# Kernel optimization log

Measured on AMD Instinct MI355X. Metric: run time of the kernel, lower is better.

## Reference

```python
import jax, jax.numpy as jnp
import numpy as np

FORGET_RADIX = 10
HIDDEN_RADIX = 23
LN2 = float(np.log(2.0))
MAX_FORGET = 0.875
BATCH, IN_SIZE, H_SIZE = 8192, 1024, 2048
G = H_SIZE // 2  # group size (h_size // 2)


def setup_inputs() -> dict:
    key = jax.random.key(0)
    ks = jax.random.split(key, 6)
    x = jax.random.normal(ks[0], (BATCH, IN_SIZE), dtype=jnp.float32)
    # hidden is a fixed-point (radix 23) int state; values correspond to floats in (-0.125, 0.125)
    hidden = jax.random.randint(ks[1], (BATCH, H_SIZE), -(2**20), 2**20, dtype=jnp.int32)

    def lin(k, fan_in, fan_out):
        kw, kb = jax.random.split(k)
        s = 1.0 / np.sqrt(fan_in)
        W = jax.random.uniform(kw, (fan_in, fan_out), jnp.float32, -s, s)
        b = jax.random.uniform(kb, (fan_out,), jnp.float32, -s, s)
        return W, b

    W_zr1, b_zr1 = lin(ks[2], IN_SIZE + G, H_SIZE)
    W_g1, b_g1 = lin(ks[3], IN_SIZE + G, G)
    W_zr2, b_zr2 = lin(ks[4], IN_SIZE + G, H_SIZE)
    W_g2, b_g2 = lin(ks[5], IN_SIZE + G, G)
    return {"x": x, "hidden": hidden,
            "W_zr1": W_zr1, "b_zr1": b_zr1, "W_g1": W_g1, "b_g1": b_g1,
            "W_zr2": W_zr2, "b_zr2": b_zr2, "W_g2": W_g2, "b_g2": b_g2,
            "slice_dim": 0}


def _to_float(h_fix, radix):
    # ConvertToFloat: fixed-point int -> float
    return h_fix.astype(jnp.float32) / np.float32(2.0 ** radix)


def _to_fixed(v, radix):
    # ConvertToFixed: float -> fixed-point int (truncation toward zero, like Tensor.int())
    return jnp.trunc(v * np.float32(2.0 ** radix)).astype(jnp.int64)


def reference(x, hidden, W_zr1, b_zr1, W_g1, b_g1, W_zr2, b_zr2, W_g2, b_g2, slice_dim):
    h = hidden.astype(jnp.int64)  # widen so h * z_fix (up to ~2^34) does not overflow
    h1, h2 = h[:, :G], h[:, G:]

    # ---- group 1 update (reads h2) ----
    h2_fl = _to_float(h2, HIDDEN_RADIX)
    zr1 = jax.nn.sigmoid(jnp.concatenate([x, h2_fl], axis=1) @ W_zr1 + b_zr1)
    z1, r1 = zr1[:, :G], zr1[:, G:]
    z1 = MAX_FORGET * z1 + (1.0 - MAX_FORGET)
    g1 = jnp.tanh(jnp.concatenate([x, r1 * h2_fl], axis=1) @ W_g1 + b_g1)
    z1_fix = jnp.maximum(_to_fixed(z1, FORGET_RADIX), 1)  # EnsureNotForgetAll
    h1 = jnp.floor_divide(h1 * z1_fix, 2 ** FORGET_RADIX)  # FixedMultiply, buf=None, mask=1
    h1 = h1 + _to_fixed((1.0 - z1) * g1, HIDDEN_RADIX)     # + MaskFixedMultiply(update1, 1)

    # ---- group 2 update (reads updated h1) ----
    h1_fl = _to_float(h1, HIDDEN_RADIX)
    zr2 = jax.nn.sigmoid(jnp.concatenate([x, h1_fl], axis=1) @ W_zr2 + b_zr2)
    z2, r2 = zr2[:, :G], zr2[:, G:]
    z2 = MAX_FORGET * z2 + (1.0 - MAX_FORGET)
    g2 = jnp.tanh(jnp.concatenate([x, r2 * h1_fl], axis=1) @ W_g2 + b_g2)
    z2_fix = jnp.maximum(_to_fixed(z2, FORGET_RADIX), 1)
    h2 = jnp.floor_divide(h2 * z2_fix, 2 ** FORGET_RADIX)
    h2 = h2 + _to_fixed((1.0 - z2) * g2, HIDDEN_RADIX)

    recurrent_hidden = jnp.concatenate([h1, h2], axis=1).astype(jnp.int32)
    output_hidden = recurrent_hidden.astype(jnp.float32) / np.float32(2.0 ** HIDDEN_RADIX)

    optimal_bits = (jnp.sum(-jnp.log(z1[:, slice_dim:]) / LN2)
                    + jnp.sum(-jnp.log(z2) / LN2)
                    + 32.0 * slice_dim * x.shape[0])
    return recurrent_hidden, output_hidden, optimal_bits
```

## Files before the change

### kernel.cpp

```cpp
#include <hip/hip_runtime.h>
#include <hip/hip_bf16.h>

#define BATCH   8192
#define IN_SZ   1024
#define HSZ     2048
#define GG      1024
#define KTOT    2048

typedef __hip_bfloat16 bf16;
typedef __attribute__((ext_vector_type(8))) short  short8;
typedef __attribute__((ext_vector_type(4))) float  floatx4;

typedef __attribute__((address_space(1))) const void gvoid_t;
typedef __attribute__((address_space(3))) void       lvoid_t;

__device__ __forceinline__ void async_ld16(void* lds, const void* g) {
  __builtin_amdgcn_global_load_lds((gvoid_t*)g, (lvoid_t*)lds, 16, 0, 0);
}

__global__ void prep_all(const float* __restrict__ x, bf16* __restrict__ xb,
                         const int* __restrict__ hidden, bf16* __restrict__ hf,
                         float* accp,
                         const float* __restrict__ W_zr1, const float* __restrict__ W_g1,
                         const float* __restrict__ W_zr2, const float* __restrict__ W_g2,
                         bf16* __restrict__ wt_zr1, bf16* __restrict__ wt_g1,
                         bf16* __restrict__ wt_zr2, bf16* __restrict__ wt_g2) {
  int b = blockIdx.x;
  int t = threadIdx.x;
  if (b < 3072) {
    const float* W; bf16* Wt; int N; int tb = b;
    if (tb < 1024)      { W = W_zr1; Wt = wt_zr1; N = 2048; }
    else if (tb < 1536) { W = W_g1;  Wt = wt_g1;  N = 1024; tb -= 1024; }
    else if (tb < 2560) { W = W_zr2; Wt = wt_zr2; N = 2048; tb -= 1536; }
    else                { W = W_g2;  Wt = wt_g2;  N = 1024; tb -= 2560; }
    int ntn = N >> 6;
    int k0 = (tb / ntn) * 64, n0 = (tb % ntn) * 64;
    __shared__ float tile[64][65];
    int kk = t >> 4, nn = (t & 15) * 4;
#pragma unroll
    for (int s = 0; s < 4; ++s) {
      int row = kk + s * 16;
      float4 v = *(const float4*)&W[(size_t)(k0 + row) * N + n0 + nn];
      tile[row][nn + 0] = v.x; tile[row][nn + 1] = v.y;
      tile[row][nn + 2] = v.z; tile[row][nn + 3] = v.w;
    }
    __syncthreads();
    int k8 = (t & 7) * 8;
#pragma unroll
    for (int s = 0; s < 2; ++s) {
      int nl = (t >> 3) + s * 32;
      bf16 vals[8];
#pragma unroll
      for (int u = 0; u < 8; ++u) vals[u] = __float2bfloat16(tile[k8 + u][nl]);
      *(short8*)&Wt[(size_t)(n0 + nl) * KTOT + k0 + k8] = *(short8*)vals;
    }
  } else {
    int idx = (b - 3072) * 256 + t;
    int i = idx * 4;
    float4 xv = *(const float4*)(x + i);
    xb[i + 0] = __float2bfloat16(xv.x);
    xb[i + 1] = __float2bfloat16(xv.y);
    xb[i + 2] = __float2bfloat16(xv.z);
    xb[i + 3] = __float2bfloat16(xv.w);
    int m = i >> 10, j = i & 1023;
    int4 hv = *(const int4*)(hidden + m * HSZ + GG + j);
    const float sc = 1.0f / 8388608.0f;
    hf[i + 0] = __float2bfloat16((float)hv.x * sc);
    hf[i + 1] = __float2bfloat16((float)hv.y * sc);
    hf[i + 2] = __float2bfloat16((float)hv.z * sc);
    hf[i + 3] = __float2bfloat16((float)hv.w * sc);
    if (idx == 0) *accp = 0.0f;
  }
}

template<int BM, int MI>
__device__ __forceinline__ void gemm_mainloop(const bf16* __restrict__ Aleft,
                                              const bf16* __restrict__ Aright,
                                              const bf16* __restrict__ Bt,
                                              bf16* As, bf16* Bs,
                                              int m0, int n0, floatx4 (&acc)[MI][4]) {
  int t = threadIdx.x;
  int r = t >> 2;
  int c2 = (t & 3) ^ ((t >> 3) & 3);
  int lane = t & 63;
  int q = lane >> 4, r16 = lane & 15;
  int w = t >> 6;
  int wm = w & 1, wn = w >> 1;
  int swz = q ^ ((r16 >> 1) & 3);

  const size_t arow0 = (size_t)(m0 + r) * IN_SZ;
  const size_t arow1 = (size_t)(m0 + r + 64) * IN_SZ;
  const size_t brow0 = (size_t)(n0 + r) * KTOT;
  const size_t brow1 = (size_t)(n0 + r + 64) * KTOT;
  bf16* lA0 = As + t * 8;
  bf16* lA1 = As + 64 * 32 + t * 8;
  bf16* lB0 = Bs + t * 8;
  bf16* lB1 = Bs + 64 * 32 + t * 8;
  const bf16* aRd = As + (wm * (BM / 2) + r16) * 32 + swz * 8;
  const bf16* bRd = Bs + (wn * 64 + r16) * 32 + swz * 8;

  for (int kb = 0; kb < KTOT / 32; ++kb) {
    int kt = kb * 32;
    const bf16* asrc; int kloc;
    if (kt < IN_SZ) { asrc = Aleft;  kloc = kt; }
    else            { asrc = Aright; kloc = kt - IN_SZ; }
    int ac = kloc + c2 * 8;
    async_ld16(lA0, asrc + arow0 + ac);
    if (BM == 128) async_ld16(lA1, asrc + arow1 + ac);
    int bc = kt + c2 * 8;
    async_ld16(lB0, Bt + brow0 + bc);
    async_ld16(lB1, Bt + brow1 + bc);
    __syncthreads();
    short8 af[MI], bfr[4];
#pragma unroll
    for (int i = 0; i < MI; ++i) af[i]  = *(const short8*)(const void*)(aRd + i * 16 * 32);
#pragma unroll
    for (int j = 0; j < 4; ++j)  bfr[j] = *(const short8*)(const void*)(bRd + j * 16 * 32);
#pragma unroll
    for (int i = 0; i < MI; ++i)
#pragma unroll
      for (int j = 0; j < 4; ++j)
        acc[i][j] = __builtin_amdgcn_mfma_f32_16x16x32_bf16(af[i], bfr[j], acc[i][j], 0, 0, 0);
    __syncthreads();
  }
}

__global__ void gemm_zr(const bf16* __restrict__ xb, const bf16* __restrict__ hfp,
                        const bf16* __restrict__ Bt, const float* __restrict__ bias,
                        bf16* __restrict__ zbuf, bf16* __restrict__ rh,
                        const int* __restrict__ slice_ptr, int use_slice,
                        float* __restrict__ accp) {
  __shared__ bf16 As[128 * 32];
  __shared__ bf16 Bs[128 * 32];
  floatx4 acc[4][4];
#pragma unroll
  for (int i = 0; i < 4; ++i)
#pragma unroll
    for (int j = 0; j < 4; ++j) acc[i][j] = (floatx4)0.0f;

  int m0 = blockIdx.y * 128, n0 = blockIdx.x * 128;
  gemm_mainloop<128, 4>(xb, hfp, Bt, As, Bs, m0, n0, acc);

  int t = threadIdx.x;
  int lane = t & 63, q = lane >> 4, r16 = lane & 15;
  int w = t >> 6, wm = w & 1, wn = w >> 1;
  int nmin = use_slice ? *slice_ptr : 0;
  float lsum = 0.0f;

#pragma unroll
  for (int i = 0; i < 4; ++i) {
    int mbase = m0 + wm * 64 + i * 16 + q * 4;
#pragma unroll
    for (int j = 0; j < 4; ++j) {
      int n = n0 + wn * 64 + j * 16 + r16;
      float bn = bias[n];
#pragma unroll
      for (int rr = 0; rr < 4; ++rr) {
        int m = mbase + rr;
        float v = acc[i][j][rr] + bn;
        float s = 1.0f / (1.0f + __expf(-v));
        if (n < GG) {
          float z = 0.875f * s + 0.125f;
          zbuf[(size_t)m * GG + n] = __float2bfloat16(z);
          if (n >= nmin) lsum += -__log2f(z);
        } else {
          int jc = n - GG;
          float hfl = __bfloat162float(hfp[(size_t)m * GG + jc]);
          rh[(size_t)m * GG + jc] = __float2bfloat16(s * hfl);
        }
      }
    }
  }
  __syncthreads();
  float* sf = (float*)As;
#pragma unroll
  for (int off = 32; off > 0; off >>= 1) lsum += __shfl_down(lsum, off, 64);
  if (lane == 0) sf[w] = lsum;
  __syncthreads();
  if (t == 0) atomicAdd(accp, sf[0] + sf[1] + sf[2] + sf[3]);
}

__global__ void gemm_g(const bf16* __restrict__ xb, const bf16* __restrict__ rh,
                       const bf16* __restrict__ Bt, const float* __restrict__ bias,
                       const bf16* __restrict__ zbuf, const int* __restrict__ hidden,
                       int col_off,
                       float* __restrict__ out0, float* __restrict__ out1,
                       bf16* __restrict__ hf_out, int write_hf,
                       int write_bits, const float* __restrict__ accp,
                       const int* __restrict__ slice_ptr, float* __restrict__ out2) {
  __shared__ bf16 As[64 * 32];
  __shared__ bf16 Bs[128 * 32];
  floatx4 acc[2][4];
#pragma unroll
  for (int i = 0; i < 2; ++i)
#pragma unroll
    for (int j = 0; j < 4; ++j) acc[i][j] = (floatx4)0.0f;

  int m0 = blockIdx.y * 64, n0 = blockIdx.x * 128;
  gemm_mainloop<64, 2>(xb, rh, Bt, As, Bs, m0, n0, acc);

  int t = threadIdx.x;
  int lane = t & 63, q = lane >> 4, r16 = lane & 15;
  int w = t >> 6, wm = w & 1, wn = w >> 1;

#pragma unroll
  for (int i = 0; i < 2; ++i) {
    int mbase = m0 + wm * 32 + i * 16 + q * 4;
#pragma unroll
    for (int j = 0; j < 4; ++j) {
      int n = n0 + wn * 64 + j * 16 + r16;
      float bn = bias[n];
#pragma unroll
      for (int rr = 0; rr < 4; ++rr) {
        int m = mbase + rr;
        float v = acc[i][j][rr] + bn;
        float e = __expf(2.0f * v);
        float g = 1.0f - 2.0f / (e + 1.0f);
        float z = __bfloat162float(zbuf[(size_t)m * GG + n]);
        int zfix = (int)(z * 1024.0f);
        if (zfix < 1) zfix = 1;
        long long h = hidden[(size_t)m * HSZ + col_off + n];
        long long hupd = (h * (long long)zfix) >> 10;
        float t2 = (1.0f - z) * g * 8388608.0f;
        long long f2 = (long long)t2;
        int hnew = (int)(hupd + f2);
        size_t oidx = (size_t)m * HSZ + col_off + n;
        out0[oidx] = (float)hnew;
        float ofl = (float)hnew * (1.0f / 8388608.0f);
        out1[oidx] = ofl;
        if (write_hf) hf_out[(size_t)m * GG + n] = __float2bfloat16(ofl);
      }
    }
  }
  if (write_bits && blockIdx.x == 0 && blockIdx.y == 0 && t == 0) {
    *out2 = *accp + 32.0f * (float)(*slice_ptr) * (float)BATCH;
  }
}

extern "C" void kernel_launch(void* const* d_in, const int* in_sizes, int n_in,
                              void* d_out, int out_size, void* d_ws, size_t ws_size,
                              hipStream_t stream) {
  const float* x      = (const float*)d_in[0];
  const int*   hidden = (const int*)d_in[1];
  const float* W_zr1  = (const float*)d_in[2];
  const float* b_zr1  = (const float*)d_in[3];
  const float* W_g1   = (const float*)d_in[4];
  const float* b_g1   = (const float*)d_in[5];
  const float* W_zr2  = (const float*)d_in[6];
  const float* b_zr2  = (const float*)d_in[7];
  const float* W_g2   = (const float*)d_in[8];
  const float* b_g2   = (const float*)d_in[9];
  const int*   slice  = (const int*)d_in[10];

  char* ws = (char*)d_ws;
  size_t off = 0;
  auto alloc = [&](size_t bytes) -> void* {
    void* p = ws + off;
    off += (bytes + 255) & ~(size_t)255;
    return p;
  };
  bf16* xb     = (bf16*)alloc((size_t)BATCH * IN_SZ * 2);
  bf16* wt_zr1 = (bf16*)alloc((size_t)2048 * 2048 * 2);
  bf16* wt_g1  = (bf16*)alloc((size_t)1024 * 2048 * 2);
  bf16* wt_zr2 = (bf16*)alloc((size_t)2048 * 2048 * 2);
  bf16* wt_g2  = (bf16*)alloc((size_t)1024 * 2048 * 2);
  bf16* hf     = (bf16*)alloc((size_t)BATCH * GG * 2);
  bf16* rh     = (bf16*)alloc((size_t)BATCH * GG * 2);
  bf16* zbuf   = (bf16*)alloc((size_t)BATCH * GG * 2);
  float* accp  = (float*)alloc(256);

  float* out0 = (float*)d_out;
  float* out1 = out0 + (size_t)BATCH * HSZ;
  float* out2 = out0 + 2 * (size_t)BATCH * HSZ;

  prep_all<<<3072 + 8192, 256, 0, stream>>>(x, xb, hidden, hf, accp,
                                            W_zr1, W_g1, W_zr2, W_g2,
                                            wt_zr1, wt_g1, wt_zr2, wt_g2);

  gemm_zr<<<dim3(16, 64), 256, 0, stream>>>(xb, hf, wt_zr1, b_zr1, zbuf, rh, slice, 1, accp);
  gemm_g<<<dim3(8, 128), 256, 0, stream>>>(xb, rh, wt_g1, b_g1, zbuf, hidden, 0,
                                           out0, out1, hf, 1, 0, accp, slice, out2);
  gemm_zr<<<dim3(16, 64), 256, 0, stream>>>(xb, hf, wt_zr2, b_zr2, zbuf, rh, slice, 0, accp);
  gemm_g<<<dim3(8, 128), 256, 0, stream>>>(xb, rh, wt_g2, b_g2, zbuf, hidden, 1024,
                                           out0, out1, hf, 0, 1, accp, slice, out2);
}
```

Measured before the change: 644.3 us.

## Double GEMM K-step to 64, reshape g tiles, and remap blocks M-major

The GEMM main loop now stages 64-wide K slices in LDS instead of 32, with a new XOR swizzle over 8 chunks, which halves the number of barrier pairs per K sweep. The gate GEMM changes its tile from 64x128 to 128x64. Both kernels map block indices so consecutive blocks walk along M while sharing an N tile, aiming for better L2 reuse of weights. Larger LDS footprints (32 KB for zr) together with launch_bounds occupancy hints may limit residency.

```diff
diff --git a/kernel.cpp b/kernel.cpp
--- a/kernel.cpp
+++ b/kernel.cpp
@@ -73,73 +73,87 @@
   }
 }
 
-template<int BM, int MI>
+template<int BM, int BN, int MI, int NJ>
 __device__ __forceinline__ void gemm_mainloop(const bf16* __restrict__ Aleft,
                                               const bf16* __restrict__ Aright,
                                               const bf16* __restrict__ Bt,
                                               bf16* As, bf16* Bs,
-                                              int m0, int n0, floatx4 (&acc)[MI][4]) {
+                                              int m0, int n0, floatx4 (&acc)[MI][NJ]) {
+  constexpr int ACALLS = BM / 32;
+  constexpr int BCALLS = BN / 32;
   int t = threadIdx.x;
-  int r = t >> 2;
-  int c2 = (t & 3) ^ ((t >> 3) & 3);
   int lane = t & 63;
+  int w = t >> 6;
+  int l3 = lane >> 3;
+  int gchunk = (lane & 7) ^ l3;
+  int rbase = w * 8 + l3;
   int q = lane >> 4, r16 = lane & 15;
-  int w = t >> 6;
   int wm = w & 1, wn = w >> 1;
-  int swz = q ^ ((r16 >> 1) & 3);
-
-  const size_t arow0 = (size_t)(m0 + r) * IN_SZ;
-  const size_t arow1 = (size_t)(m0 + r + 64) * IN_SZ;
-  const size_t brow0 = (size_t)(n0 + r) * KTOT;
-  const size_t brow1 = (size_t)(n0 + r + 64) * KTOT;
-  bf16* lA0 = As + t * 8;
-  bf16* lA1 = As + 64 * 32 + t * 8;
-  bf16* lB0 = Bs + t * 8;
-  bf16* lB1 = Bs + 64 * 32 + t * 8;
-  const bf16* aRd = As + (wm * (BM / 2) + r16) * 32 + swz * 8;
-  const bf16* bRd = Bs + (wn * 64 + r16) * 32 + swz * 8;
-
-  for (int kb = 0; kb < KTOT / 32; ++kb) {
-    int kt = kb * 32;
+
+  size_t a_off[ACALLS], b_off[BCALLS];
+  bf16 *lA[ACALLS], *lB[BCALLS];
+#pragma unroll
+  for (int s = 0; s < ACALLS; ++s) {
+    a_off[s] = (size_t)(m0 + rbase + s * 32) * IN_SZ + gchunk * 8;
+    lA[s] = As + (s * 32 + w * 8) * 64 + lane * 8;
+  }
+#pragma unroll
+  for (int s = 0; s < BCALLS; ++s) {
+    b_off[s] = (size_t)(n0 + rbase + s * 32) * KTOT + gchunk * 8;
+    lB[s] = Bs + (s * 32 + w * 8) * 64 + lane * 8;
+  }
+  const bf16* aRdBase = As + (wm * (BM / 2) + r16) * 64;
+  const bf16* bRdBase = Bs + (wn * (BN / 2) + r16) * 64;
+  int pc[2];
+  pc[0] = ((q) ^ (r16 & 7)) * 8;
+  pc[1] = ((4 + q) ^ (r16 & 7)) * 8;
+
+  for (int kb = 0; kb < KTOT / 64; ++kb) {
+    int kt = kb * 64;
     const bf16* asrc; int kloc;
     if (kt < IN_SZ) { asrc = Aleft;  kloc = kt; }
     else            { asrc = Aright; kloc = kt - IN_SZ; }
-    int ac = kloc + c2 * 8;
-    async_ld16(lA0, asrc + arow0 + ac);
-    if (BM == 128) async_ld16(lA1, asrc + arow1 + ac);
-    int bc = kt + c2 * 8;
-    async_ld16(lB0, Bt + brow0 + bc);
-    async_ld16(lB1, Bt + brow1 + bc);
+#pragma unroll
+    for (int s = 0; s < ACALLS; ++s) async_ld16(lA[s], asrc + a_off[s] + kloc);
+#pragma unroll
+    for (int s = 0; s < BCALLS; ++s) async_ld16(lB[s], Bt + b_off[s] + kt);
     __syncthreads();
-    short8 af[MI], bfr[4];
-#pragma unroll
-    for (int i = 0; i < MI; ++i) af[i]  = *(const short8*)(const void*)(aRd + i * 16 * 32);
-#pragma unroll
-    for (int j = 0; j < 4; ++j)  bfr[j] = *(const short8*)(const void*)(bRd + j * 16 * 32);
-#pragma unroll
-    for (int i = 0; i < MI; ++i)
-#pragma unroll
-      for (int j = 0; j < 4; ++j)
-        acc[i][j] = __builtin_amdgcn_mfma_f32_16x16x32_bf16(af[i], bfr[j], acc[i][j], 0, 0, 0);
+#pragma unroll
+    for (int kh = 0; kh < 2; ++kh) {
+      short8 af[MI], bfr[NJ];
+#pragma unroll
+      for (int i = 0; i < MI; ++i)
+        af[i]  = *(const short8*)(const void*)(aRdBase + i * 16 * 64 + pc[kh]);
+#pragma unroll
+      for (int j = 0; j < NJ; ++j)
+        bfr[j] = *(const short8*)(const void*)(bRdBase + j * 16 * 64 + pc[kh]);
+#pragma unroll
+      for (int i = 0; i < MI; ++i)
+#pragma unroll
+        for (int j = 0; j < NJ; ++j)
+          acc[i][j] = __builtin_amdgcn_mfma_f32_16x16x32_bf16(af[i], bfr[j], acc[i][j], 0, 0, 0);
+    }
     __syncthreads();
   }
 }
 
-__global__ void gemm_zr(const bf16* __restrict__ xb, const bf16* __restrict__ hfp,
-                        const bf16* __restrict__ Bt, const float* __restrict__ bias,
-                        bf16* __restrict__ zbuf, bf16* __restrict__ rh,
-                        const int* __restrict__ slice_ptr, int use_slice,
-                        float* __restrict__ accp) {
-  __shared__ bf16 As[128 * 32];
-  __shared__ bf16 Bs[128 * 32];
+__global__ void __launch_bounds__(256, 4)
+gemm_zr(const bf16* __restrict__ xb, const bf16* __restrict__ hfp,
+        const bf16* __restrict__ Bt, const float* __restrict__ bias,
+        bf16* __restrict__ zbuf, bf16* __restrict__ rh,
+        const int* __restrict__ slice_ptr, int use_slice,
+        float* __restrict__ accp) {
+  __shared__ bf16 As[128 * 64];
+  __shared__ bf16 Bs[128 * 64];
   floatx4 acc[4][4];
 #pragma unroll
   for (int i = 0; i < 4; ++i)
 #pragma unroll
     for (int j = 0; j < 4; ++j) acc[i][j] = (floatx4)0.0f;
 
-  int m0 = blockIdx.y * 128, n0 = blockIdx.x * 128;
-  gemm_mainloop<128, 4>(xb, hfp, Bt, As, Bs, m0, n0, acc);
+  int linear = blockIdx.y * gridDim.x + blockIdx.x;
+  int m0 = (linear & 63) * 128, n0 = (linear >> 6) * 128;
+  gemm_mainloop<128, 128, 4, 4>(xb, hfp, Bt, As, Bs, m0, n0, acc);
 
   int t = threadIdx.x;
   int lane = t & 63, q = lane >> 4, r16 = lane & 15;
@@ -180,35 +194,37 @@
   if (t == 0) atomicAdd(accp, sf[0] + sf[1] + sf[2] + sf[3]);
 }
 
-__global__ void gemm_g(const bf16* __restrict__ xb, const bf16* __restrict__ rh,
-                       const bf16* __restrict__ Bt, const float* __restrict__ bias,
-                       const bf16* __restrict__ zbuf, const int* __restrict__ hidden,
-                       int col_off,
-                       float* __restrict__ out0, float* __restrict__ out1,
-                       bf16* __restrict__ hf_out, int write_hf,
-                       int write_bits, const float* __restrict__ accp,
-                       const int* __restrict__ slice_ptr, float* __restrict__ out2) {
-  __shared__ bf16 As[64 * 32];
-  __shared__ bf16 Bs[128 * 32];
-  floatx4 acc[2][4];
-#pragma unroll
-  for (int i = 0; i < 2; ++i)
-#pragma unroll
-    for (int j = 0; j < 4; ++j) acc[i][j] = (floatx4)0.0f;
-
-  int m0 = blockIdx.y * 64, n0 = blockIdx.x * 128;
-  gemm_mainloop<64, 2>(xb, rh, Bt, As, Bs, m0, n0, acc);
+__global__ void __launch_bounds__(256, 4)
+gemm_g(const bf16* __restrict__ xb, const bf16* __restrict__ rh,
+       const bf16* __restrict__ Bt, const float* __restrict__ bias,
+       const bf16* __restrict__ zbuf, const int* __restrict__ hidden,
+       int col_off,
+       float* __restrict__ out0, float* __restrict__ out1,
+       bf16* __restrict__ hf_out, int write_hf,
+       int write_bits, const float* __restrict__ accp,
+       const int* __restrict__ slice_ptr, float* __restrict__ out2) {
+  __shared__ bf16 As[128 * 64];
+  __shared__ bf16 Bs[64 * 64];
+  floatx4 acc[4][2];
+#pragma unroll
+  for (int i = 0; i < 4; ++i)
+#pragma unroll
+    for (int j = 0; j < 2; ++j) acc[i][j] = (floatx4)0.0f;
+
+  int linear = blockIdx.y * gridDim.x + blockIdx.x;
+  int m0 = (linear & 63) * 128, n0 = (linear >> 6) * 64;
+  gemm_mainloop<128, 64, 4, 2>(xb, rh, Bt, As, Bs, m0, n0, acc);
 
   int t = threadIdx.x;
   int lane = t & 63, q = lane >> 4, r16 = lane & 15;
   int w = t >> 6, wm = w & 1, wn = w >> 1;
 
 #pragma unroll
-  for (int i = 0; i < 2; ++i) {
-    int mbase = m0 + wm * 32 + i * 16 + q * 4;
-#pragma unroll
-    for (int j = 0; j < 4; ++j) {
-      int n = n0 + wn * 64 + j * 16 + r16;
+  for (int i = 0; i < 4; ++i) {
+    int mbase = m0 + wm * 64 + i * 16 + q * 4;
+#pragma unroll
+    for (int j = 0; j < 2; ++j) {
+      int n = n0 + wn * 32 + j * 16 + r16;
       float bn = bias[n];
 #pragma unroll
       for (int rr = 0; rr < 4; ++rr) {
@@ -278,9 +294,9 @@
                                             wt_zr1, wt_g1, wt_zr2, wt_g2);
 
   gemm_zr<<<dim3(16, 64), 256, 0, stream>>>(xb, hf, wt_zr1, b_zr1, zbuf, rh, slice, 1, accp);
-  gemm_g<<<dim3(8, 128), 256, 0, stream>>>(xb, rh, wt_g1, b_g1, zbuf, hidden, 0,
+  gemm_g<<<dim3(16, 64), 256, 0, stream>>>(xb, rh, wt_g1, b_g1, zbuf, hidden, 0,
                                            out0, out1, hf, 1, 0, accp, slice, out2);
   gemm_zr<<<dim3(16, 64), 256, 0, stream>>>(xb, hf, wt_zr2, b_zr2, zbuf, rh, slice, 0, accp);
-  gemm_g<<<dim3(8, 128), 256, 0, stream>>>(xb, rh, wt_g2, b_g2, zbuf, hidden, 1024,
+  gemm_g<<<dim3(16, 64), 256, 0, stream>>>(xb, rh, wt_g2, b_g2, zbuf, hidden, 1024,
                                            out0, out1, hf, 0, 1, accp, slice, out2);
 }
```

Result: faster. 560.9 us (-12.9%).
